# Kernel optimization log

Hardware: AMD Instinct MI355X
Metric: run time of the kernel (lower is better)

Reference implementation:

```python
import jax, jax.numpy as jnp
import numpy as np
import math

T, N, D, H = 1024, 8, 1024, 16
HD = D // H  # head_dim = 64


def setup_inputs() -> dict:
    key = jax.random.key(0)
    k1, k2, k3, k4 = jax.random.split(key, 4)
    scale = 1.0 / math.sqrt(D)  # roughly xavier-scale params
    return {
        "x": jax.random.normal(k1, (T, N, D), dtype=jnp.float32),
        "q_weight": jax.random.normal(k2, (D, H, HD), dtype=jnp.float32) * scale,
        "v_weight": jax.random.normal(k3, (D, H, HD), dtype=jnp.float32) * scale,
        "out_w": jax.random.normal(k4, (D, D), dtype=jnp.float32) * scale,
        "out_b": jnp.zeros((D,), dtype=jnp.float32),
    }


def reference(x, q_weight, v_weight, out_w, out_b):
    inv_sqrt_hd = 1.0 / math.sqrt(HD)
    # q = k : (T, N, H, HD)
    q = jnp.einsum('tbm,mhd->tbhd', x, q_weight)
    q_sq = jnp.einsum('tbhd,tbhd->tbh', q, q)  # squared norms
    # squared L2 distance logits: (T, S, N, H)
    squared_dist = q_sq[:, None] + q_sq[None, :] - 2.0 * jnp.einsum('tbhd,sbhd->tsbh', q, q)
    attn_logits = -squared_dist * inv_sqrt_hd
    attn_weights = jax.nn.softmax(attn_logits, axis=1)  # softmax over source dim S
    # A = W_q W_q^T per head: (H, D, D)
    A = jnp.einsum('mhd,nhd->hmn', q_weight, q_weight) * inv_sqrt_hd
    XA = jnp.einsum('tbm,hmn->tbhn', x, A)           # (T, N, H, D)
    PXA = jnp.einsum('tsbh,sbhm->tbhm', attn_weights, XA)  # (T, N, H, D)
    PXAV = jnp.einsum('tbhm,mhd->tbhd', PXA, v_weight).reshape(T, N, D)
    return PXAV @ out_w.T + out_b
```

## Files before the change

### kernel.cpp

```cpp
#include <hip/hip_runtime.h>
#include <hip/hip_bf16.h>

#define T_ 1024
#define N_ 8
#define D_ 1024
#define H_ 16
#define HD_ 64

typedef __attribute__((ext_vector_type(8))) short bf16x8;
typedef __attribute__((ext_vector_type(4))) float f32x4;
typedef __attribute__((ext_vector_type(16))) float f32x16;
typedef __attribute__((ext_vector_type(4))) int i32x4;
typedef __attribute__((ext_vector_type(2))) int i32x2;
typedef unsigned short u16;
typedef unsigned int u32;

__device__ __forceinline__ float bf2f(u16 u){
  union { float f; unsigned int i; } v; v.i = ((unsigned int)u) << 16; return v.f;
}
__device__ __forceinline__ u16 f2bf(float f){
  union { float f; unsigned int i; } v; v.f = f;
  unsigned int r = v.i + 0x7FFFu + ((v.i >> 16) & 1u);
  return (u16)(r >> 16);
}
__device__ __forceinline__ u16 f2bf_fast(float f){
  __hip_bfloat16 h = __float2bfloat16(f);
  return *reinterpret_cast<u16*>(&h);
}
__device__ __forceinline__ float exp2_raw(float x){
  float r;
  asm("v_exp_f32 %0, %1" : "=v"(r) : "v"(x));
  return r;
}
__device__ __forceinline__ void gl_lds16(const u16* g, u16* l){
  __builtin_amdgcn_global_load_lds(
      (const __attribute__((address_space(1))) unsigned int*)g,
      (__attribute__((address_space(3))) unsigned int*)(unsigned int)(unsigned long long)l,
      16, 0, 0);
}

__global__ __launch_bounds__(256) void k_wqt(const float* __restrict__ Wq, u16* __restrict__ Wqt){
  __shared__ float tld[64][65];
  int m0 = blockIdx.x * 64, n0 = blockIdx.y * 64;
  int col = threadIdx.x & 63, rq = threadIdx.x >> 6;
  #pragma unroll
  for (int p = 0; p < 16; ++p){
    int row = rq * 16 + p;
    tld[row][col] = Wq[(size_t)(m0 + row) * D_ + n0 + col];
  }
  __syncthreads();
  #pragma unroll
  for (int p = 0; p < 16; ++p){
    int row = rq * 16 + p;
    Wqt[(size_t)(n0 + row) * D_ + m0 + col] = f2bf(tld[col][row]);
  }
}

__global__ __launch_bounds__(256) void k_bmatp(const float* __restrict__ qw, const float* __restrict__ vw,
                                               float* __restrict__ Bp){
  int h = (int)blockIdx.x >> 3, sp = (int)blockIdx.x & 7;
  int tid = threadIdx.x, lane = tid & 63, w = tid >> 6;
  int g = lane >> 4, c = lane & 15;
  __shared__ u16 Qt[64 * 72];
  __shared__ u16 Vt[64 * 72];
  f32x4 zero = {0.f, 0.f, 0.f, 0.f};
  f32x4 acc[4];
  #pragma unroll
  for (int eb = 0; eb < 4; ++eb) acc[eb] = zero;
  int m = tid >> 2, cg = tid & 3;
  for (int mt = sp * 128; mt < sp * 128 + 128; mt += 64){
    __syncthreads();
    #pragma unroll
    for (int q = 0; q < 4; ++q){
      int e0 = cg * 16 + q * 4;
      f32x4 vq = *(const f32x4*)(qw + (size_t)(mt + m) * D_ + h * 64 + e0);
      f32x4 vv = *(const f32x4*)(vw + (size_t)(mt + m) * D_ + h * 64 + e0);
      #pragma unroll
      for (int j = 0; j < 4; ++j){
        Qt[(e0 + j) * 72 + m] = f2bf_fast(vq[j]);
        Vt[(e0 + j) * 72 + m] = f2bf_fast(vv[j]);
      }
    }
    __syncthreads();
    #pragma unroll
    for (int kk = 0; kk < 2; ++kk){
      bf16x8 av = *(const bf16x8*)&Vt[(w * 16 + c) * 72 + kk * 32 + g * 8];
      #pragma unroll
      for (int eb = 0; eb < 4; ++eb){
        bf16x8 bq = *(const bf16x8*)&Qt[(eb * 16 + c) * 72 + kk * 32 + g * 8];
        acc[eb] = __builtin_amdgcn_mfma_f32_16x16x32_bf16(av, bq, acc[eb], 0, 0, 0);
      }
    }
  }
  #pragma unroll
  for (int eb = 0; eb < 4; ++eb)
    #pragma unroll
    for (int r = 0; r < 4; ++r){
      int d = w * 16 + g * 4 + r, e = eb * 16 + c;
      Bp[(((size_t)sp * 16 + h) * 64 + d) * 64 + e] = acc[eb][r];
    }
}

__global__ __launch_bounds__(256) void k_bred(const float* __restrict__ Bp, u16* __restrict__ Bt){
  int i = blockIdx.x * 256 + threadIdx.x;
  float s = 0.f;
  #pragma unroll
  for (int j = 0; j < 8; ++j) s += Bp[(size_t)j * 65536 + i];
  Bt[i] = f2bf(s * 0.125f);
}

__device__ __forceinline__ int swz(int row, int colbyte){
  return row * 64 + (((colbyte) ^ ((row & 7) << 4)) >> 1);
}

template<int A_F32, int B_F32, int EPI>
__global__ __launch_bounds__(256) void k_gemm(const void* __restrict__ A_, const void* __restrict__ B_,
                                              void* __restrict__ Cv, const float* __restrict__ bias,
                                              int M, int N, int K){
  int nbn = N >> 7;
  int ii = (int)blockIdx.x;
  int sw = (ii & 7) * 64 + (ii >> 3);
  int bm = sw / nbn, bn = sw % nbn;
  int tid = threadIdx.x, lane = tid & 63, wid = tid >> 6;
  int wr = wid >> 1, wc = wid & 1, g = lane >> 4, c = lane & 15;
  __shared__ u16 As[128 * 64];
  __shared__ u16 Bs[128 * 64];
  int srow[4], scol[4], sdst[4];
  #pragma unroll
  for (int p = 0; p < 4; ++p){
    int slot = (wid * 4 + p) * 64 + lane;
    int row = slot >> 3, c8 = slot & 7;
    srow[p] = row;
    scol[p] = (c8 ^ (row & 7)) * 8;
    sdst[p] = slot * 8;
  }
  f32x4 zero = {0.f, 0.f, 0.f, 0.f};
  f32x4 acc[4][4];
  #pragma unroll
  for (int m = 0; m < 4; ++m)
    #pragma unroll
    for (int n = 0; n < 4; ++n) acc[m][n] = zero;
  for (int kt = 0; kt < K; kt += 64){
    __syncthreads();
    if (!A_F32){
      const u16* A = (const u16*)A_;
      #pragma unroll
      for (int p = 0; p < 4; ++p)
        gl_lds16(A + (size_t)(bm * 128 + srow[p]) * K + kt + scol[p], &As[sdst[p]]);
    }
    if (!B_F32){
      const u16* B = (const u16*)B_;
      #pragma unroll
      for (int p = 0; p < 4; ++p)
        gl_lds16(B + (size_t)(bn * 128 + srow[p]) * K + kt + scol[p], &Bs[sdst[p]]);
    }
    if (A_F32){
      const float* A = (const float*)A_;
      #pragma unroll
      for (int p = 0; p < 4; ++p){
        int ci = tid + p * 256;
        int row = ci >> 3, c8 = ci & 7;
        const float* src = A + (size_t)(bm * 128 + row) * K + kt + c8 * 8;
        f32x4 v0 = *(const f32x4*)src;
        f32x4 v1 = *(const f32x4*)(src + 4);
        union { u16 u[8]; i32x4 v; } pk;
        #pragma unroll
        for (int j = 0; j < 4; ++j){ pk.u[j] = f2bf_fast(v0[j]); pk.u[4 + j] = f2bf_fast(v1[j]); }
        *(i32x4*)&As[swz(row, c8 * 16)] = pk.v;
      }
    }
    if (B_F32){
      const float* B = (const float*)B_;
      #pragma unroll
      for (int p = 0; p < 4; ++p){
        int ci = tid + p * 256;
        int row = ci >> 3, c8 = ci & 7;
        const float* src = B + (size_t)(bn * 128 + row) * K + kt + c8 * 8;
        f32x4 v0 = *(const f32x4*)src;
        f32x4 v1 = *(const f32x4*)(src + 4);
        union { u16 u[8]; i32x4 v; } pk;
        #pragma unroll
        for (int j = 0; j < 4; ++j){ pk.u[j] = f2bf_fast(v0[j]); pk.u[4 + j] = f2bf_fast(v1[j]); }
        *(i32x4*)&Bs[swz(row, c8 * 16)] = pk.v;
      }
    }
    __syncthreads();
    #pragma unroll
    for (int kk = 0; kk < 2; ++kk){
      bf16x8 af[4], bfr[4];
      #pragma unroll
      for (int m = 0; m < 4; ++m){
        int row = wr * 64 + m * 16 + c;
        af[m] = *(const bf16x8*)&As[swz(row, kk * 64 + g * 16)];
      }
      #pragma unroll
      for (int n = 0; n < 4; ++n){
        int row = wc * 64 + n * 16 + c;
        bfr[n] = *(const bf16x8*)&Bs[swz(row, kk * 64 + g * 16)];
      }
      #pragma unroll
      for (int m = 0; m < 4; ++m)
        #pragma unroll
        for (int n = 0; n < 4; ++n)
          acc[m][n] = __builtin_amdgcn_mfma_f32_16x16x32_bf16(af[m], bfr[n], acc[m][n], 0, 0, 0);
    }
  }
  #pragma unroll
  for (int m = 0; m < 4; ++m)
    #pragma unroll
    for (int n = 0; n < 4; ++n)
      #pragma unroll
      for (int r = 0; r < 4; ++r){
        int row = bm * 128 + wr * 64 + m * 16 + g * 4 + r;
        int col = bn * 128 + wc * 64 + n * 16 + c;
        float v = acc[m][n][r];
        if (EPI == 0){
          int t = row >> 3, b = row & 7, hh = col >> 6, dd = col & 63;
          ((u16*)Cv)[(((size_t)(b * H_ + hh)) * T_ + t) * HD_ + dd] = f2bf(v);
        } else {
          ((float*)Cv)[(size_t)row * N + col] = v + bias[col];
        }
      }
}

__global__ __launch_bounds__(64) void k_u(const u16* __restrict__ qb, const u16* __restrict__ Bt,
                                          u16* __restrict__ ubt, float* __restrict__ qsq){
  int bh = blockIdx.x >> 4, tt = blockIdx.x & 15;
  int h = bh & 15, t0 = tt * 64;
  int lane = threadIdx.x, g = lane >> 4, c = lane & 15;
  const float QS_SCALE = 0.125f * 1.44269504088896340736f;
  bf16x8 af[4][2], bq[4][2];
  #pragma unroll
  for (int mf = 0; mf < 4; ++mf)
    #pragma unroll
    for (int kk = 0; kk < 2; ++kk)
      af[mf][kk] = *(const bf16x8*)(Bt + ((size_t)(h * 64 + mf * 16 + c)) * 64 + kk * 32 + g * 8);
  #pragma unroll
  for (int nf = 0; nf < 4; ++nf)
    #pragma unroll
    for (int kk = 0; kk < 2; ++kk)
      bq[nf][kk] = *(const bf16x8*)(qb + ((size_t)(bh * 1024 + t0 + nf * 16 + c)) * 64 + kk * 32 + g * 8);
  #pragma unroll
  for (int nf = 0; nf < 4; ++nf){
    float ss = 0.f;
    #pragma unroll
    for (int kk = 0; kk < 2; ++kk)
      #pragma unroll
      for (int j = 0; j < 8; ++j){ float f = bf2f((u16)bq[nf][kk][j]); ss = fmaf(f, f, ss); }
    ss += __shfl_xor(ss, 16);
    ss += __shfl_xor(ss, 32);
    if (lane < 16) qsq[(size_t)bh * 1024 + t0 + nf * 16 + lane] = ss * QS_SCALE;
  }
  f32x4 zero = {0.f, 0.f, 0.f, 0.f};
  f32x4 acc[4][4];
  #pragma unroll
  for (int mf = 0; mf < 4; ++mf)
    #pragma unroll
    for (int nf = 0; nf < 4; ++nf) acc[mf][nf] = zero;
  #pragma unroll
  for (int kk = 0; kk < 2; ++kk)
    #pragma unroll
    for (int mf = 0; mf < 4; ++mf)
      #pragma unroll
      for (int nf = 0; nf < 4; ++nf)
        acc[mf][nf] = __builtin_amdgcn_mfma_f32_16x16x32_bf16(af[mf][kk], bq[nf][kk], acc[mf][nf], 0, 0, 0);
  #pragma unroll
  for (int mf = 0; mf < 4; ++mf)
    #pragma unroll
    for (int nf = 0; nf < 4; ++nf)
      #pragma unroll
      for (int r = 0; r < 4; ++r)
        ubt[((size_t)(bh * 64 + mf * 16 + g * 4 + r)) * 1024 + t0 + nf * 16 + c] = f2bf(acc[mf][nf][r]);
}

__global__ __launch_bounds__(256, 4) void k_attn(const u16* __restrict__ qb, const u16* __restrict__ ubt,
                                                 const float* __restrict__ qsq, u16* __restrict__ obm){
  int i = (int)blockIdx.x;
  int bh = ((i & 7) << 4) + (i >> 6);
  int tt = (i >> 3) & 7;
  int b = bh >> 4, h = bh & 15;
  int tid = threadIdx.x, w = tid >> 6, lane = tid & 63;
  int lo = lane & 31, hi = lane >> 5;
  __shared__ u16 Kl[2][64 * 64];
  __shared__ u16 Ul[2][64 * 64];
  __shared__ float Qs[1024];
  const float C1 = 0.25f * 1.44269504088896340736f;
  int t0 = tt * 128 + w * 32;
  const u16* qbh = qb + (size_t)bh * 65536;
  const u16* ubh = ubt + (size_t)bh * 65536;
  const float* qsb = qsq + (size_t)bh * 1024;
  *(f32x4*)&Qs[tid * 4] = *(const f32x4*)(qsb + tid * 4);
  bf16x8 qB[4];
  #pragma unroll
  for (int kd = 0; kd < 4; ++kd)
    qB[kd] = *(const bf16x8*)(qbh + (t0 + lo) * 64 + kd * 16 + hi * 8);
  f32x16 o0 = {0,0,0,0,0,0,0,0,0,0,0,0,0,0,0,0};
  f32x16 o1 = {0,0,0,0,0,0,0,0,0,0,0,0,0,0,0,0};
  const f32x16 zero16 = {0,0,0,0,0,0,0,0,0,0,0,0,0,0,0,0};
  float l_c = 0.f;
  int slot0 = (w * 2 + 0) * 64 + lane, slot1 = (w * 2 + 1) * 64 + lane;
  int r0 = slot0 >> 3, sc0 = ((slot0 & 7) ^ (r0 & 7)) * 8;
  int r1 = slot1 >> 3, sc1 = ((slot1 & 7) ^ (r1 & 7)) * 8;
  int d0 = (w * 2 + 0) * 512, d1 = (w * 2 + 1) * 512;
  gl_lds16(qbh + r0 * 64 + sc0, &Kl[0][d0]);
  gl_lds16(qbh + r1 * 64 + sc1, &Kl[0][d1]);
  gl_lds16(ubh + (size_t)r0 * 1024 + sc0, &Ul[0][d0]);
  gl_lds16(ubh + (size_t)r1 * 1024 + sc1, &Ul[0][d1]);
  int cur = 0;
  for (int st = 0; st < 16; ++st){
    int s0 = st * 64;
    __syncthreads();
    if (st < 15){
      int s1 = s0 + 64;
      int nb = cur ^ 1;
      gl_lds16(qbh + (s1 + r0) * 64 + sc0, &Kl[nb][d0]);
      gl_lds16(qbh + (s1 + r1) * 64 + sc1, &Kl[nb][d1]);
      gl_lds16(ubh + (size_t)r0 * 1024 + s1 + sc0, &Ul[nb][d0]);
      gl_lds16(ubh + (size_t)r1 * 1024 + s1 + sc1, &Ul[nb][d1]);
    }
    const u16* Kc = &Kl[cur][0];
    const u16* Uc = &Ul[cur][0];
    #pragma unroll
    for (int ts = 0; ts < 2; ++ts){
      f32x16 sf = zero16;
      __builtin_amdgcn_s_setprio(1);
      #pragma unroll
      for (int kd = 0; kd < 4; ++kd){
        bf16x8 kA = *(const bf16x8*)&Kc[swz(ts * 32 + lo, kd * 32 + hi * 16)];
        sf = __builtin_amdgcn_mfma_f32_32x32x16_bf16(kA, qB[kd], sf, 0, 0, 0);
      }
      __builtin_amdgcn_s_setprio(0);
      f32x4 qs_[4];
      #pragma unroll
      for (int q = 0; q < 4; ++q)
        qs_[q] = *(const f32x4*)&Qs[s0 + ts * 32 + q * 8 + hi * 4];
      float p[16];
      #pragma unroll
      for (int r = 0; r < 16; ++r)
        p[r] = exp2_raw(fmaf(sf[r], C1, -qs_[r >> 2][r & 3]));
      float sA = ((p[0] + p[1]) + (p[2] + p[3])) + ((p[4] + p[5]) + (p[6] + p[7]));
      float sB = ((p[8] + p[9]) + (p[10] + p[11])) + ((p[12] + p[13]) + (p[14] + p[15]));
      l_c += sA + sB;
      u32 W[8];
      #pragma unroll
      for (int q = 0; q < 8; ++q)
        W[q] = ((u32)f2bf_fast(p[2 * q + 1]) << 16) | (u32)f2bf_fast(p[2 * q]);
      #pragma unroll
      for (int ml = 0; ml < 2; ++ml){
        int m_g = ts * 2 + ml;
        int base = ml * 4;
        i32x2 sw0 = __builtin_amdgcn_permlane32_swap((int)W[base + 0], (int)W[base + 2], false, false);
        i32x2 sw1 = __builtin_amdgcn_permlane32_swap((int)W[base + 1], (int)W[base + 3], false, false);
        union { u32 wd[4]; bf16x8 v; } pa;
        pa.wd[0] = (u32)sw0[0]; pa.wd[1] = (u32)sw1[0]; pa.wd[2] = (u32)sw0[1]; pa.wd[3] = (u32)sw1[1];
        bf16x8 u0 = *(const bf16x8*)&Uc[swz(lo, m_g * 32 + hi * 16)];
        bf16x8 u1 = *(const bf16x8*)&Uc[swz(32 + lo, m_g * 32 + hi * 16)];
        __builtin_amdgcn_s_setprio(1);
        o0 = __builtin_amdgcn_mfma_f32_32x32x16_bf16(pa.v, u0, o0, 0, 0, 0);
        o1 = __builtin_amdgcn_mfma_f32_32x32x16_bf16(pa.v, u1, o1, 0, 0, 0);
        __builtin_amdgcn_s_setprio(0);
      }
    }
    cur ^= 1;
  }
  l_c += __shfl_xor(l_c, 32);
  float inv = 1.0f / l_c;
  #pragma unroll
  for (int r = 0; r < 16; ++r){
    int tr = (r & 3) + 8 * (r >> 2) + 4 * hi;
    float invr = __shfl(inv, tr);
    size_t rowb = ((size_t)((t0 + tr) * 8 + b)) * 1024 + h * 64;
    obm[rowb + lo] = f2bf(o0[r] * invr);
    obm[rowb + 32 + lo] = f2bf(o1[r] * invr);
  }
}

extern "C" void kernel_launch(void* const* d_in, const int* in_sizes, int n_in,
                              void* d_out, int out_size, void* d_ws, size_t ws_size,
                              hipStream_t stream) {
  const float* x   = (const float*)d_in[0];
  const float* qw  = (const float*)d_in[1];
  const float* vw  = (const float*)d_in[2];
  const float* ow  = (const float*)d_in[3];
  const float* ob_bias = (const float*)d_in[4];
  float* out = (float*)d_out;

  float* Bp = (float*)d_out;
  u16* qb  = (u16*)d_out;
  u16* ubt = (u16*)((char*)d_out + (size_t)16 * 1024 * 1024);

  char* ws = (char*)d_ws;
  size_t off = 0;
  auto alloc = [&](size_t bytes) -> void* {
    void* p = ws + off;
    off += (bytes + 255) & ~(size_t)255;
    return p;
  };
  u16*   wqt = (u16*)  alloc((size_t)1024 * 1024 * 2);
  u16*   obm = (u16*)  alloc((size_t)8192 * 1024 * 2);
  float* qsq = (float*)alloc((size_t)128 * 1024 * 4);
  u16*   Bt  = (u16*)  alloc((size_t)16 * 64 * 64 * 2);

  k_bmatp<<<128, 256, 0, stream>>>(qw, vw, Bp);
  k_bred<<<256, 256, 0, stream>>>(Bp, Bt);
  k_wqt<<<dim3(16, 16), 256, 0, stream>>>(qw, wqt);
  k_gemm<1, 0, 0><<<512, 256, 0, stream>>>(x, wqt, qb, nullptr, 8192, 1024, 1024);
  k_u<<<2048, 64, 0, stream>>>(qb, Bt, ubt, qsq);
  k_attn<<<1024, 256, 0, stream>>>(qb, ubt, qsq, obm);
  k_gemm<0, 1, 1><<<512, 256, 0, stream>>>(obm, ow, out, ob_bias, 8192, 1024, 1024);
}
```

Baseline: 135.7 us.

## Double-buffer GEMM LDS tiles with register prefetch; pack k_u into 256-thread blocks

The GEMM kernel now uses two LDS buffers per operand. While MFMAs run on the current buffer, the next K-tile is prefetched, either by async global-to-LDS loads for bf16 operands or into registers for fp32 operands, which are converted and stored after compute. This is meant to hide global load latency, and it drops one barrier per iteration. Separately, k_u launches 512 blocks of 4 waves instead of 2048 single-wave blocks to cut per-block overhead. The extra LDS (64KB) and prefetch registers may lower occupancy.

```diff
diff --git a/kernel.cpp b/kernel.cpp
--- a/kernel.cpp
+++ b/kernel.cpp
@@ -123,8 +123,8 @@
   int bm = sw / nbn, bn = sw % nbn;
   int tid = threadIdx.x, lane = tid & 63, wid = tid >> 6;
   int wr = wid >> 1, wc = wid & 1, g = lane >> 4, c = lane & 15;
-  __shared__ u16 As[128 * 64];
-  __shared__ u16 Bs[128 * 64];
+  __shared__ u16 As[2][128 * 64];
+  __shared__ u16 Bs[2][128 * 64];
   int srow[4], scol[4], sdst[4];
   #pragma unroll
   for (int p = 0; p < 4; ++p){
@@ -134,69 +134,109 @@
     scol[p] = (c8 ^ (row & 7)) * 8;
     sdst[p] = slot * 8;
   }
+  int rrow[4], rc8[4];
+  #pragma unroll
+  for (int p = 0; p < 4; ++p){
+    int ci = tid + p * 256;
+    rrow[p] = ci >> 3; rc8[p] = ci & 7;
+  }
   f32x4 zero = {0.f, 0.f, 0.f, 0.f};
   f32x4 acc[4][4];
   #pragma unroll
   for (int m = 0; m < 4; ++m)
     #pragma unroll
     for (int n = 0; n < 4; ++n) acc[m][n] = zero;
-  for (int kt = 0; kt < K; kt += 64){
+  f32x4 rA[4][2], rB[4][2];
+  const u16* Ab = (const u16*)A_;
+  const u16* Bb = (const u16*)B_;
+  const float* Af = (const float*)A_;
+  const float* Bf = (const float*)B_;
+  if (!A_F32){
+    #pragma unroll
+    for (int p = 0; p < 4; ++p)
+      gl_lds16(Ab + (size_t)(bm * 128 + srow[p]) * K + scol[p], &As[0][sdst[p]]);
+  }
+  if (!B_F32){
+    #pragma unroll
+    for (int p = 0; p < 4; ++p)
+      gl_lds16(Bb + (size_t)(bn * 128 + srow[p]) * K + scol[p], &Bs[0][sdst[p]]);
+  }
+  if (A_F32){
+    #pragma unroll
+    for (int p = 0; p < 4; ++p){
+      const float* src = Af + (size_t)(bm * 128 + rrow[p]) * K + rc8[p] * 8;
+      rA[p][0] = *(const f32x4*)src;
+      rA[p][1] = *(const f32x4*)(src + 4);
+    }
+    #pragma unroll
+    for (int p = 0; p < 4; ++p){
+      union { u16 u[8]; i32x4 v; } pk;
+      #pragma unroll
+      for (int j = 0; j < 4; ++j){ pk.u[j] = f2bf_fast(rA[p][0][j]); pk.u[4 + j] = f2bf_fast(rA[p][1][j]); }
+      *(i32x4*)&As[0][swz(rrow[p], rc8[p] * 16)] = pk.v;
+    }
+  }
+  if (B_F32){
+    #pragma unroll
+    for (int p = 0; p < 4; ++p){
+      const float* src = Bf + (size_t)(bn * 128 + rrow[p]) * K + rc8[p] * 8;
+      rB[p][0] = *(const f32x4*)src;
+      rB[p][1] = *(const f32x4*)(src + 4);
+    }
+    #pragma unroll
+    for (int p = 0; p < 4; ++p){
+      union { u16 u[8]; i32x4 v; } pk;
+      #pragma unroll
+      for (int j = 0; j < 4; ++j){ pk.u[j] = f2bf_fast(rB[p][0][j]); pk.u[4 + j] = f2bf_fast(rB[p][1][j]); }
+      *(i32x4*)&Bs[0][swz(rrow[p], rc8[p] * 16)] = pk.v;
+    }
+  }
+  int NT = K >> 6;
+  int cur = 0;
+  for (int st = 0; st < NT; ++st){
     __syncthreads();
-    if (!A_F32){
-      const u16* A = (const u16*)A_;
-      #pragma unroll
-      for (int p = 0; p < 4; ++p)
-        gl_lds16(A + (size_t)(bm * 128 + srow[p]) * K + kt + scol[p], &As[sdst[p]]);
-    }
-    if (!B_F32){
-      const u16* B = (const u16*)B_;
-      #pragma unroll
-      for (int p = 0; p < 4; ++p)
-        gl_lds16(B + (size_t)(bn * 128 + srow[p]) * K + kt + scol[p], &Bs[sdst[p]]);
-    }
-    if (A_F32){
-      const float* A = (const float*)A_;
-      #pragma unroll
-      for (int p = 0; p < 4; ++p){
-        int ci = tid + p * 256;
-        int row = ci >> 3, c8 = ci & 7;
-        const float* src = A + (size_t)(bm * 128 + row) * K + kt + c8 * 8;
-        f32x4 v0 = *(const f32x4*)src;
-        f32x4 v1 = *(const f32x4*)(src + 4);
-        union { u16 u[8]; i32x4 v; } pk;
-        #pragma unroll
-        for (int j = 0; j < 4; ++j){ pk.u[j] = f2bf_fast(v0[j]); pk.u[4 + j] = f2bf_fast(v1[j]); }
-        *(i32x4*)&As[swz(row, c8 * 16)] = pk.v;
-      }
-    }
-    if (B_F32){
-      const float* B = (const float*)B_;
-      #pragma unroll
-      for (int p = 0; p < 4; ++p){
-        int ci = tid + p * 256;
-        int row = ci >> 3, c8 = ci & 7;
-        const float* src = B + (size_t)(bn * 128 + row) * K + kt + c8 * 8;
-        f32x4 v0 = *(const f32x4*)src;
-        f32x4 v1 = *(const f32x4*)(src + 4);
-        union { u16 u[8]; i32x4 v; } pk;
-        #pragma unroll
-        for (int j = 0; j < 4; ++j){ pk.u[j] = f2bf_fast(v0[j]); pk.u[4 + j] = f2bf_fast(v1[j]); }
-        *(i32x4*)&Bs[swz(row, c8 * 16)] = pk.v;
-      }
-    }
-    __syncthreads();
+    int kt1 = (st + 1) * 64;
+    int nb = cur ^ 1;
+    if (st + 1 < NT){
+      if (!A_F32){
+        #pragma unroll
+        for (int p = 0; p < 4; ++p)
+          gl_lds16(Ab + (size_t)(bm * 128 + srow[p]) * K + kt1 + scol[p], &As[nb][sdst[p]]);
+      }
+      if (!B_F32){
+        #pragma unroll
+        for (int p = 0; p < 4; ++p)
+          gl_lds16(Bb + (size_t)(bn * 128 + srow[p]) * K + kt1 + scol[p], &Bs[nb][sdst[p]]);
+      }
+      if (A_F32){
+        #pragma unroll
+        for (int p = 0; p < 4; ++p){
+          const float* src = Af + (size_t)(bm * 128 + rrow[p]) * K + kt1 + rc8[p] * 8;
+          rA[p][0] = *(const f32x4*)src;
+          rA[p][1] = *(const f32x4*)(src + 4);
+        }
+      }
+      if (B_F32){
+        #pragma unroll
+        for (int p = 0; p < 4; ++p){
+          const float* src = Bf + (size_t)(bn * 128 + rrow[p]) * K + kt1 + rc8[p] * 8;
+          rB[p][0] = *(const f32x4*)src;
+          rB[p][1] = *(const f32x4*)(src + 4);
+        }
+      }
+    }
     #pragma unroll
     for (int kk = 0; kk < 2; ++kk){
       bf16x8 af[4], bfr[4];
       #pragma unroll
       for (int m = 0; m < 4; ++m){
         int row = wr * 64 + m * 16 + c;
-        af[m] = *(const bf16x8*)&As[swz(row, kk * 64 + g * 16)];
+        af[m] = *(const bf16x8*)&As[cur][swz(row, kk * 64 + g * 16)];
       }
       #pragma unroll
       for (int n = 0; n < 4; ++n){
         int row = wc * 64 + n * 16 + c;
-        bfr[n] = *(const bf16x8*)&Bs[swz(row, kk * 64 + g * 16)];
+        bfr[n] = *(const bf16x8*)&Bs[cur][swz(row, kk * 64 + g * 16)];
       }
       #pragma unroll
       for (int m = 0; m < 4; ++m)
@@ -204,6 +244,27 @@
         for (int n = 0; n < 4; ++n)
           acc[m][n] = __builtin_amdgcn_mfma_f32_16x16x32_bf16(af[m], bfr[n], acc[m][n], 0, 0, 0);
     }
+    if (st + 1 < NT){
+      if (A_F32){
+        #pragma unroll
+        for (int p = 0; p < 4; ++p){
+          union { u16 u[8]; i32x4 v; } pk;
+          #pragma unroll
+          for (int j = 0; j < 4; ++j){ pk.u[j] = f2bf_fast(rA[p][0][j]); pk.u[4 + j] = f2bf_fast(rA[p][1][j]); }
+          *(i32x4*)&As[nb][swz(rrow[p], rc8[p] * 16)] = pk.v;
+        }
+      }
+      if (B_F32){
+        #pragma unroll
+        for (int p = 0; p < 4; ++p){
+          union { u16 u[8]; i32x4 v; } pk;
+          #pragma unroll
+          for (int j = 0; j < 4; ++j){ pk.u[j] = f2bf_fast(rB[p][0][j]); pk.u[4 + j] = f2bf_fast(rB[p][1][j]); }
+          *(i32x4*)&Bs[nb][swz(rrow[p], rc8[p] * 16)] = pk.v;
+        }
+      }
+    }
+    cur ^= 1;
   }
   #pragma unroll
   for (int m = 0; m < 4; ++m)
@@ -223,11 +284,14 @@
       }
 }
 
-__global__ __launch_bounds__(64) void k_u(const u16* __restrict__ qb, const u16* __restrict__ Bt,
-                                          u16* __restrict__ ubt, float* __restrict__ qsq){
-  int bh = blockIdx.x >> 4, tt = blockIdx.x & 15;
+__global__ __launch_bounds__(256) void k_u(const u16* __restrict__ qb, const u16* __restrict__ Bt,
+                                           u16* __restrict__ ubt, float* __restrict__ qsq){
+  int blk = (int)blockIdx.x;
+  int bh = blk >> 2;
+  int w = threadIdx.x >> 6;
+  int tt = (blk & 3) * 4 + w;
   int h = bh & 15, t0 = tt * 64;
-  int lane = threadIdx.x, g = lane >> 4, c = lane & 15;
+  int lane = threadIdx.x & 63, g = lane >> 4, c = lane & 15;
   const float QS_SCALE = 0.125f * 1.44269504088896340736f;
   bf16x8 af[4][2], bq[4][2];
   #pragma unroll
@@ -405,7 +469,7 @@
   k_bred<<<256, 256, 0, stream>>>(Bp, Bt);
   k_wqt<<<dim3(16, 16), 256, 0, stream>>>(qw, wqt);
   k_gemm<1, 0, 0><<<512, 256, 0, stream>>>(x, wqt, qb, nullptr, 8192, 1024, 1024);
-  k_u<<<2048, 64, 0, stream>>>(qb, Bt, ubt, qsq);
+  k_u<<<512, 256, 0, stream>>>(qb, Bt, ubt, qsq);
   k_attn<<<1024, 256, 0, stream>>>(qb, ubt, qsq, obm);
   k_gemm<0, 1, 1><<<512, 256, 0, stream>>>(obm, ow, out, ob_bias, 8192, 1024, 1024);
 }
```

Measured after the change: 127.8 us. 5.8% less time.
